# Kernel optimization log

Hardware: AMD Instinct MI355X
Metric: run time of the kernel (lower is better)

Reference implementation:

```python
import jax, jax.numpy as jnp
import numpy as np

B, T, E = 8, 1048576, 8
C, K, S = 128, 512, 512


def setup_inputs() -> dict:
    key = jax.random.key(0)
    k1, k2, k3, k4, k5 = jax.random.split(key, 5)
    fan = 1.0 / np.sqrt(E * K)  # torch Conv1d default init range
    z = jax.random.normal(k1, (B, T, E), dtype=jnp.float32)
    W1 = jax.random.uniform(k2, (C, E, K), dtype=jnp.float32, minval=-fan, maxval=fan)
    b1 = jax.random.uniform(k3, (C,), dtype=jnp.float32, minval=-fan, maxval=fan)
    W2 = jax.random.uniform(k4, (C, E, K), dtype=jnp.float32, minval=-fan, maxval=fan)
    b2 = jax.random.uniform(k5, (C,), dtype=jnp.float32, minval=-fan, maxval=fan)
    return {"z": z, "W1": W1, "b1": b1, "W2": W2, "b2": b2}


def _conv1d(x_bct, w_oik, b_o):
    # x: (B, E, T), w: (C, E, K), stride S, VALID padding -> (B, C, L)
    y = jax.lax.conv_general_dilated(
        x_bct, w_oik, window_strides=(S,), padding="VALID",
        dimension_numbers=("NCH", "OIH", "NCH"))
    return y + b_o[None, :, None]


def reference(z, W1, b1, W2, b2):
    zt = jnp.transpose(z, (0, 2, 1))          # (B, E, T)
    c1 = _conv1d(zt, W1, b1)                  # (B, C, L)
    c2 = _conv1d(zt, W2, b2)
    g = c1 * jax.nn.sigmoid(c2)               # gated conv
    return jnp.max(g, axis=-1)                # global max-over-time -> (B, C)
```

## Files before the change

kernel.cpp:

```cpp
#include <hip/hip_runtime.h>
#include <hip/hip_bf16.h>
#include <stdint.h>

typedef __attribute__((ext_vector_type(8))) short short8;
typedef __attribute__((ext_vector_type(4))) float f32x4;

#define NT 64
#define NBUF 4

typedef const __attribute__((address_space(1))) unsigned int* gas_ptr;
typedef __attribute__((address_space(3))) unsigned int* las_ptr;

__device__ __forceinline__ void gload_lds16(const void* g, void* l) {
  __builtin_amdgcn_global_load_lds((gas_ptr)g, (las_ptr)l, 16, 0, 0);
}

__device__ __forceinline__ unsigned pack_bf2(float a, float b) {
  union { __hip_bfloat162 h2; unsigned u; } cv;
  cv.h2 = __float22bfloat162_rn(make_float2(a, b));
  return cv.u;
}

__device__ __forceinline__ short8 pack8(const f32x4& a, const f32x4& b) {
  union { unsigned u[4]; short8 s; } cv;
  cv.u[0] = pack_bf2(a.x, a.y); cv.u[1] = pack_bf2(a.z, a.w);
  cv.u[2] = pack_bf2(b.x, b.y); cv.u[3] = pack_bf2(b.z, b.w);
  return cv.s;
}

__global__ void pack_w(const float* __restrict__ W1, const float* __restrict__ W2,
                       __hip_bfloat16* __restrict__ WB) {
  int idx = blockIdx.x * 256 + threadIdx.x;
  int kk = idx & 4095, n = idx >> 12;
  int k = kk >> 3, e = kk & 7, c = n >> 1;
  const float* W = (n & 1) ? W2 : W1;
  WB[(size_t)n * 4096 + kk] = __float2bfloat16(W[(c * 8 + e) * 512 + k]);
}

__global__ __launch_bounds__(256, 2) void gemm_gate(
    const float* __restrict__ z, const __hip_bfloat16* __restrict__ WB,
    const float* __restrict__ b1, const float* __restrict__ b2,
    float* __restrict__ partial) {
  __shared__ __align__(16) char Bs[NBUF][16384];

  const int t = threadIdx.x;
  const int l = t & 63, w = t >> 6;
  const int wm = w >> 1, wn = w & 1;
  const int lr = l & 15, lk = l >> 4;

  const int h = blockIdx.x;
  const int logical = (h & 7) * 64 + (h >> 3);
  const int mb = logical >> 1, nh = logical & 1;

  const int rowbase = mb * 64 + wm * 32;
  const int nbase = nh * 128;

  const char* bsrc[4];
#pragma unroll
  for (int r = 0; r < 4; ++r) {
    int col = r * 32 + (t >> 3);
    int inner = ((t & 7) * 16) ^ ((col & 7) << 4);
    bsrc[r] = (const char*)(WB + (size_t)(nbase + col) * 4096) + inner;
  }

  const char* abase = (const char*)(z + (size_t)(rowbase + lr) * 4096 + lk * 8);

  f32x4 acc[2][4];
#pragma unroll
  for (int i = 0; i < 2; ++i)
#pragma unroll
    for (int j = 0; j < 4; ++j) acc[i][j] = (f32x4)0.0f;

  f32x4 acur[8], anext[8];

#pragma unroll
  for (int kt0 = 0; kt0 < 3; ++kt0)
#pragma unroll
    for (int r = 0; r < 4; ++r)
      gload_lds16(bsrc[r] + (size_t)kt0 * 128, &Bs[kt0][r * 4096 + t * 16]);
#pragma unroll
  for (int mi = 0; mi < 2; ++mi)
#pragma unroll
    for (int ks = 0; ks < 2; ++ks)
#pragma unroll
      for (int hf = 0; hf < 2; ++hf)
        acur[mi * 4 + ks * 2 + hf] =
            *(const f32x4*)(abase + ((size_t)mi * 16 * 4096 + ks * 32 + hf * 4) * 4);
  asm volatile("s_waitcnt vmcnt(0)" ::: "memory");
  __builtin_amdgcn_s_barrier();

  const int swz = (lr & 7) << 4;
#pragma unroll 1
  for (int kt = 0; kt < NT; ++kt) {
    if (kt + 3 < NT) {
      char* dst = (char*)Bs[(kt + 3) & 3];
#pragma unroll
      for (int r = 0; r < 4; ++r)
        gload_lds16(bsrc[r] + (size_t)(kt + 3) * 128, dst + r * 4096 + t * 16);
    }
    if (kt + 1 < NT) {
#pragma unroll
      for (int mi = 0; mi < 2; ++mi)
#pragma unroll
        for (int ks = 0; ks < 2; ++ks)
#pragma unroll
          for (int hf = 0; hf < 2; ++hf)
            anext[mi * 4 + ks * 2 + hf] = *(const f32x4*)(
                abase + ((size_t)(kt + 1) * 64 + (size_t)mi * 16 * 4096 + ks * 32 + hf * 4) * 4);
    }
    short8 af[2][2];
#pragma unroll
    for (int mi = 0; mi < 2; ++mi)
#pragma unroll
      for (int ks = 0; ks < 2; ++ks)
        af[mi][ks] = pack8(acur[mi * 4 + ks * 2], acur[mi * 4 + ks * 2 + 1]);
    const char* bb = (const char*)Bs[kt & 3];
    short8 bf[4][2];
#pragma unroll
    for (int nj = 0; nj < 4; ++nj) {
      const int col = wn * 64 + nj * 16 + lr;
#pragma unroll
      for (int ks = 0; ks < 2; ++ks)
        bf[nj][ks] = *(const short8*)(bb + col * 128 + ((ks * 64 + lk * 16) ^ swz));
    }
#pragma unroll
    for (int mi = 0; mi < 2; ++mi)
#pragma unroll
      for (int nj = 0; nj < 4; ++nj)
#pragma unroll
        for (int ks = 0; ks < 2; ++ks)
          acc[mi][nj] = __builtin_amdgcn_mfma_f32_16x16x32_bf16(
              af[mi][ks], bf[nj][ks], acc[mi][nj], 0, 0, 0);
    if (kt + 1 < NT) {
#pragma unroll
      for (int i = 0; i < 8; ++i) acur[i] = anext[i];
    }
    __builtin_amdgcn_s_barrier();
  }

#pragma unroll
  for (int nj = 0; nj < 4; ++nj) {
    const int c = nh * 64 + wn * 32 + nj * 8 + (lr >> 1);
    const float vb1 = b1[c], vb2 = b2[c];
    float gm = -3.4e38f;
#pragma unroll
    for (int mi = 0; mi < 2; ++mi) {
#pragma unroll
      for (int rr = 0; rr < 4; ++rr) {
        float v = acc[mi][nj][rr];
        float p = __shfl_xor(v, 1, 64);
        float c1 = (lr & 1) ? p : v;
        float c2 = (lr & 1) ? v : p;
        c1 += vb1; c2 += vb2;
        float g = c1 * (1.0f / (1.0f + __expf(-c2)));
        gm = fmaxf(gm, g);
      }
    }
    gm = fmaxf(gm, __shfl_xor(gm, 16, 64));
    gm = fmaxf(gm, __shfl_xor(gm, 32, 64));
    if ((l < 16) && !(l & 1))
      partial[(size_t)(mb * 2 + wm) * 128 + c] = gm;
  }
}

__global__ void reduce_max(const float* __restrict__ partial, float* __restrict__ out) {
  int idx = blockIdx.x * 256 + threadIdx.x;
  if (idx >= 1024) return;
  int b = idx >> 7, c = idx & 127;
  float m = -3.4e38f;
#pragma unroll 8
  for (int g = 0; g < 64; ++g)
    m = fmaxf(m, partial[(size_t)(b * 64 + g) * 128 + c]);
  out[idx] = m;
}

extern "C" void kernel_launch(void* const* d_in, const int* in_sizes, int n_in,
                              void* d_out, int out_size, void* d_ws, size_t ws_size,
                              hipStream_t stream) {
  const float* z  = (const float*)d_in[0];
  const float* W1 = (const float*)d_in[1];
  const float* b1 = (const float*)d_in[2];
  const float* W2 = (const float*)d_in[3];
  const float* b2 = (const float*)d_in[4];
  float* out = (float*)d_out;

  __hip_bfloat16* WB = (__hip_bfloat16*)d_ws;
  float* partial = (float*)((char*)d_ws + 2 * 1024 * 1024);

  pack_w<<<4096, 256, 0, stream>>>(W1, W2, WB);
  gemm_gate<<<512, 256, 0, stream>>>(z, WB, b1, b2, partial);
  reduce_max<<<4, 256, 0, stream>>>(partial, out);
}
```

Before: 464.0 us.

## Load pre-swizzled B fragments directly from global, dropping LDS staging and barriers

The weight pack kernel now writes bf16 weights in the exact per-lane MFMA fragment order, so each lane reads its B operands straight from global/L2 with contiguous 16-byte loads. The LDS ring buffer, async global-to-LDS copies and per-iteration block barriers are removed. The main loop is unrolled by two with ping-pong register buffers for A and B to overlap loads with MFMA work. This raises register pressure and moves all B traffic onto L2 instead of sharing it through LDS across waves.

```diff
diff --git a/kernel.cpp b/kernel.cpp
--- a/kernel.cpp
+++ b/kernel.cpp
@@ -4,16 +4,6 @@
 
 typedef __attribute__((ext_vector_type(8))) short short8;
 typedef __attribute__((ext_vector_type(4))) float f32x4;
-
-#define NT 64
-#define NBUF 4
-
-typedef const __attribute__((address_space(1))) unsigned int* gas_ptr;
-typedef __attribute__((address_space(3))) unsigned int* las_ptr;
-
-__device__ __forceinline__ void gload_lds16(const void* g, void* l) {
-  __builtin_amdgcn_global_load_lds((gas_ptr)g, (las_ptr)l, 16, 0, 0);
-}
 
 __device__ __forceinline__ unsigned pack_bf2(float a, float b) {
   union { __hip_bfloat162 h2; unsigned u; } cv;
@@ -31,39 +21,73 @@
 __global__ void pack_w(const float* __restrict__ W1, const float* __restrict__ W2,
                        __hip_bfloat16* __restrict__ WB) {
   int idx = blockIdx.x * 256 + threadIdx.x;
-  int kk = idx & 4095, n = idx >> 12;
-  int k = kk >> 3, e = kk & 7, c = n >> 1;
-  const float* W = (n & 1) ? W2 : W1;
-  WB[(size_t)n * 4096 + kk] = __float2bfloat16(W[(c * 8 + e) * 512 + k]);
+  int j  = idx & 7;
+  int l  = (idx >> 3) & 63;
+  int ks = (idx >> 9) & 1;
+  int g  = (idx >> 10) & 15;
+  int kt = idx >> 14;
+  int lr = l & 15, lk = l >> 4;
+  int col = g * 16 + lr;
+  int kk = kt * 64 + ks * 32 + lk * 8 + j;
+  int c = col >> 1;
+  const float* W = (col & 1) ? W2 : W1;
+  WB[idx] = __float2bfloat16(W[(c * 8 + (kk & 7)) * 512 + (kk >> 3)]);
 }
+
+#define LOADA(dst, kt_) do { \
+  _Pragma("unroll") \
+  for (int mi = 0; mi < 2; ++mi) \
+    _Pragma("unroll") \
+    for (int ks = 0; ks < 2; ++ks) \
+      _Pragma("unroll") \
+      for (int hf = 0; hf < 2; ++hf) \
+        dst[mi*4+ks*2+hf] = *(const f32x4*)(abase + \
+            ((size_t)(kt_) * 64 + (size_t)mi * 16 * 4096 + ks * 32 + hf * 4) * 4); \
+} while (0)
+
+#define LOADB(dst, kt_) do { \
+  _Pragma("unroll") \
+  for (int nj = 0; nj < 4; ++nj) \
+    _Pragma("unroll") \
+    for (int ks = 0; ks < 2; ++ks) \
+      dst[nj*2+ks] = *(const short8*)(bbase + \
+          (size_t)(kt_) * 32768 + nj * 2048 + ks * 1024); \
+} while (0)
+
+#define COMPUTE(a_, b_) do { \
+  short8 af[2][2]; \
+  _Pragma("unroll") \
+  for (int mi = 0; mi < 2; ++mi) \
+    _Pragma("unroll") \
+    for (int ks = 0; ks < 2; ++ks) \
+      af[mi][ks] = pack8(a_[mi*4+ks*2], a_[mi*4+ks*2+1]); \
+  _Pragma("unroll") \
+  for (int mi = 0; mi < 2; ++mi) \
+    _Pragma("unroll") \
+    for (int nj = 0; nj < 4; ++nj) \
+      _Pragma("unroll") \
+      for (int ks = 0; ks < 2; ++ks) \
+        acc[mi][nj] = __builtin_amdgcn_mfma_f32_16x16x32_bf16( \
+            af[mi][ks], b_[nj*2+ks], acc[mi][nj], 0, 0, 0); \
+} while (0)
 
 __global__ __launch_bounds__(256, 2) void gemm_gate(
     const float* __restrict__ z, const __hip_bfloat16* __restrict__ WB,
     const float* __restrict__ b1, const float* __restrict__ b2,
     float* __restrict__ partial) {
-  __shared__ __align__(16) char Bs[NBUF][16384];
-
   const int t = threadIdx.x;
   const int l = t & 63, w = t >> 6;
   const int wm = w >> 1, wn = w & 1;
-  const int lr = l & 15, lk = l >> 4;
+  const int lr = l & 15;
 
   const int h = blockIdx.x;
   const int logical = (h & 7) * 64 + (h >> 3);
   const int mb = logical >> 1, nh = logical & 1;
+  const int rowbase = mb * 64 + wm * 32;
 
-  const int rowbase = mb * 64 + wm * 32;
-  const int nbase = nh * 128;
-
-  const char* bsrc[4];
-#pragma unroll
-  for (int r = 0; r < 4; ++r) {
-    int col = r * 32 + (t >> 3);
-    int inner = ((t & 7) * 16) ^ ((col & 7) << 4);
-    bsrc[r] = (const char*)(WB + (size_t)(nbase + col) * 4096) + inner;
-  }
-
-  const char* abase = (const char*)(z + (size_t)(rowbase + lr) * 4096 + lk * 8);
+  const char* abase = (const char*)(z + (size_t)(rowbase + lr) * 4096 + (l >> 4) * 8);
+  const int gbase = nh * 8 + wn * 4;
+  const char* bbase = (const char*)WB + (size_t)gbase * 2048 + (size_t)l * 16;
 
   f32x4 acc[2][4];
 #pragma unroll
@@ -71,72 +95,20 @@
 #pragma unroll
     for (int j = 0; j < 4; ++j) acc[i][j] = (f32x4)0.0f;
 
-  f32x4 acur[8], anext[8];
+  f32x4 aE[8], aO[8];
+  short8 bE[8], bO[8];
 
-#pragma unroll
-  for (int kt0 = 0; kt0 < 3; ++kt0)
-#pragma unroll
-    for (int r = 0; r < 4; ++r)
-      gload_lds16(bsrc[r] + (size_t)kt0 * 128, &Bs[kt0][r * 4096 + t * 16]);
-#pragma unroll
-  for (int mi = 0; mi < 2; ++mi)
-#pragma unroll
-    for (int ks = 0; ks < 2; ++ks)
-#pragma unroll
-      for (int hf = 0; hf < 2; ++hf)
-        acur[mi * 4 + ks * 2 + hf] =
-            *(const f32x4*)(abase + ((size_t)mi * 16 * 4096 + ks * 32 + hf * 4) * 4);
-  asm volatile("s_waitcnt vmcnt(0)" ::: "memory");
-  __builtin_amdgcn_s_barrier();
-
-  const int swz = (lr & 7) << 4;
+  LOADA(aE, 0); LOADB(bE, 0);
 #pragma unroll 1
-  for (int kt = 0; kt < NT; ++kt) {
-    if (kt + 3 < NT) {
-      char* dst = (char*)Bs[(kt + 3) & 3];
-#pragma unroll
-      for (int r = 0; r < 4; ++r)
-        gload_lds16(bsrc[r] + (size_t)(kt + 3) * 128, dst + r * 4096 + t * 16);
-    }
-    if (kt + 1 < NT) {
-#pragma unroll
-      for (int mi = 0; mi < 2; ++mi)
-#pragma unroll
-        for (int ks = 0; ks < 2; ++ks)
-#pragma unroll
-          for (int hf = 0; hf < 2; ++hf)
-            anext[mi * 4 + ks * 2 + hf] = *(const f32x4*)(
-                abase + ((size_t)(kt + 1) * 64 + (size_t)mi * 16 * 4096 + ks * 32 + hf * 4) * 4);
-    }
-    short8 af[2][2];
-#pragma unroll
-    for (int mi = 0; mi < 2; ++mi)
-#pragma unroll
-      for (int ks = 0; ks < 2; ++ks)
-        af[mi][ks] = pack8(acur[mi * 4 + ks * 2], acur[mi * 4 + ks * 2 + 1]);
-    const char* bb = (const char*)Bs[kt & 3];
-    short8 bf[4][2];
-#pragma unroll
-    for (int nj = 0; nj < 4; ++nj) {
-      const int col = wn * 64 + nj * 16 + lr;
-#pragma unroll
-      for (int ks = 0; ks < 2; ++ks)
-        bf[nj][ks] = *(const short8*)(bb + col * 128 + ((ks * 64 + lk * 16) ^ swz));
-    }
-#pragma unroll
-    for (int mi = 0; mi < 2; ++mi)
-#pragma unroll
-      for (int nj = 0; nj < 4; ++nj)
-#pragma unroll
-        for (int ks = 0; ks < 2; ++ks)
-          acc[mi][nj] = __builtin_amdgcn_mfma_f32_16x16x32_bf16(
-              af[mi][ks], bf[nj][ks], acc[mi][nj], 0, 0, 0);
-    if (kt + 1 < NT) {
-#pragma unroll
-      for (int i = 0; i < 8; ++i) acur[i] = anext[i];
-    }
-    __builtin_amdgcn_s_barrier();
+  for (int kt = 0; kt < 62; kt += 2) {
+    LOADA(aO, kt + 1); LOADB(bO, kt + 1);
+    COMPUTE(aE, bE);
+    LOADA(aE, kt + 2); LOADB(bE, kt + 2);
+    COMPUTE(aO, bO);
   }
+  LOADA(aO, 63); LOADB(bO, 63);
+  COMPUTE(aE, bE);
+  COMPUTE(aO, bO);
 
 #pragma unroll
   for (int nj = 0; nj < 4; ++nj) {
```

After: 470.3 us. No clear change (+1.4%).
